# Performance work log

Hardware: AMD Instinct MI355X
Metric: run time of the kernel (lower is better)

## Reference

```python
import jax, jax.numpy as jnp
import numpy as np

E, T, D_IN, D_HID, D_OUT = 8, 2048, 1024, 4096, 1024
INTER = 2 * D_HID  # gated (SwiGLU) -> weight1 produces [gate, val]


def setup_inputs() -> dict:
    key = jax.random.key(0)
    k_x, k_w1, k_w2 = jax.random.split(key, 3)
    # kaiming_uniform-ish scale for weights
    x = jax.random.normal(k_x, (E, T, D_IN), dtype=jnp.float32)
    w1 = jax.random.normal(k_w1, (E, D_IN, INTER), dtype=jnp.float32) * (1.0 / np.sqrt(D_IN))
    w2 = jax.random.normal(k_w2, (E, D_HID, D_OUT), dtype=jnp.float32) * (1.0 / np.sqrt(D_HID))
    return {"x": x, "weight1": w1, "weight2": w2}


def reference(x, weight1, weight2):
    # h: [E, T, 2*D_HID] grouped GEMM over experts
    h = jnp.einsum("etd,edi->eti", x, weight1)
    gate, val = jnp.split(h, 2, axis=-1)
    h = jax.nn.silu(gate) * val  # SwiGLU; dropout is identity in eval / p=0
    out = jnp.einsum("eth,eho->eto", h, weight2)  # [E, T, D_OUT]
    return out
```

## Files before the change

### kernel.cpp

```cpp
#include <hip/hip_runtime.h>


#define E_    8
#define T_    2048
#define DIN   1024
#define DHID  4096
#define DOUT  1024
#define INTER 8192

typedef _Float16 f16;
typedef _Float16 f16x8 __attribute__((ext_vector_type(8)));
typedef float    f32x4 __attribute__((ext_vector_type(4)));

typedef const __attribute__((address_space(1))) void gvoid_t;
typedef __attribute__((address_space(3))) void lvoid_t;

__device__ __forceinline__ void gload_lds16(const void* g, void* l) {
  __builtin_amdgcn_global_load_lds((gvoid_t*)g, (lvoid_t*)l, 16, 0, 0);
}

__global__ __launch_bounds__(256) void conv_f32_f16(
    const float* __restrict__ src, f16* __restrict__ dst, int n8) {
  int i = blockIdx.x * 256 + threadIdx.x;
  int stride = gridDim.x * 256;
  for (; i < n8; i += stride) {
    const float4* s = (const float4*)(src + (size_t)i * 8);
    float4 a0 = s[0], a1 = s[1];
    f16x8 v;
    v[0] = (f16)a0.x; v[1] = (f16)a0.y; v[2] = (f16)a0.z; v[3] = (f16)a0.w;
    v[4] = (f16)a1.x; v[5] = (f16)a1.y; v[6] = (f16)a1.z; v[7] = (f16)a1.w;
    *(f16x8*)(dst + (size_t)i * 8) = v;
  }
}

__global__ __launch_bounds__(256) void xpose64_f32_f16(
    const float* __restrict__ src, f16* __restrict__ dst,
    int R, int C, int tC) {
  __shared__ f16 tile[64][72];
  int bid = blockIdx.x;
  int perE = (R >> 6) * tC;
  int e = bid / perE;
  int rem = bid - e * perE;
  int rt = rem / tC;
  int ct = rem - rt * tC;
  int r0 = rt << 6, c0 = ct << 6;
  int t = threadIdx.x;
  int lr  = t >> 2;
  int lc4 = (t & 3) * 16;
  const float* s = src + (size_t)e * R * C + (size_t)(r0 + lr) * C + c0 + lc4;
#pragma unroll
  for (int i = 0; i < 4; ++i) {
    float4 v = *(const float4*)(s + i * 4);
    tile[lr][lc4 + i * 4 + 0] = (f16)v.x;
    tile[lr][lc4 + i * 4 + 1] = (f16)v.y;
    tile[lr][lc4 + i * 4 + 2] = (f16)v.z;
    tile[lr][lc4 + i * 4 + 3] = (f16)v.w;
  }
  __syncthreads();
  f16* d = dst + (size_t)e * C * R + (size_t)(c0 + lr) * R + r0 + lc4;
  f16x8 o0, o1;
#pragma unroll
  for (int j = 0; j < 8; ++j) o0[j] = tile[lc4 + j][lr];
#pragma unroll
  for (int j = 0; j < 8; ++j) o1[j] = tile[lc4 + 8 + j][lr];
  *(f16x8*)(d)     = o0;
  *(f16x8*)(d + 8) = o1;
}

__global__ __launch_bounds__(512, 2) void gemm1_swiglu_xh(
    const f16* __restrict__ xh,
    const f16* __restrict__ w1t,
    f16* __restrict__ hact) {
  __shared__ f16 As[128][32];
  __shared__ f16 Bg[128][32];
  __shared__ f16 Bv[128][32];

  int bid = blockIdx.x;
  int e   = bid >> 9;
  int rem = bid & 511;
  int mt  = rem >> 5;
  int nt  = rem & 31;
  int m0 = mt * 128, n0 = nt * 128;

  const f16* xe = xh  + ((size_t)e * T_ + m0) * DIN;
  const f16* wg = w1t + ((size_t)e * INTER + n0) * DIN;
  const f16* wv = w1t + ((size_t)e * INTER + DHID + n0) * DIN;

  int tid  = threadIdx.x;
  int lane = tid & 63;
  int wid  = tid >> 6;

  int srow = wid * 16 + (lane >> 2);
  int scol = (lane & 3) * 8;
  f16* lA = &As[wid * 16][0];
  f16* lG = &Bg[wid * 16][0];
  f16* lV = &Bv[wid * 16][0];

  int wm = wid >> 2;
  int wn = wid & 3;
  int lr = lane & 15;
  int lk = (lane >> 4) * 8;

  f32x4 accG[4][2], accV[4][2];
#pragma unroll
  for (int m = 0; m < 4; ++m)
#pragma unroll
    for (int n = 0; n < 2; ++n) {
      accG[m][n] = f32x4{0.f, 0.f, 0.f, 0.f};
      accV[m][n] = f32x4{0.f, 0.f, 0.f, 0.f};
    }

  for (int k = 0; k < DIN; k += 32) {
    __syncthreads();
    gload_lds16(xe + (size_t)srow * DIN + k + scol, lA);
    gload_lds16(wg + (size_t)srow * DIN + k + scol, lG);
    gload_lds16(wv + (size_t)srow * DIN + k + scol, lV);
    __syncthreads();

    f16x8 af[4], bg[2], bv[2];
#pragma unroll
    for (int m = 0; m < 4; ++m)
      af[m] = *(const f16x8*)&As[wm * 64 + m * 16 + lr][lk];
#pragma unroll
    for (int n = 0; n < 2; ++n) {
      bg[n] = *(const f16x8*)&Bg[wn * 32 + n * 16 + lr][lk];
      bv[n] = *(const f16x8*)&Bv[wn * 32 + n * 16 + lr][lk];
    }
#pragma unroll
    for (int m = 0; m < 4; ++m)
#pragma unroll
      for (int n = 0; n < 2; ++n) {
        accG[m][n] = __builtin_amdgcn_mfma_f32_16x16x32_f16(af[m], bg[n], accG[m][n], 0, 0, 0);
        accV[m][n] = __builtin_amdgcn_mfma_f32_16x16x32_f16(af[m], bv[n], accV[m][n], 0, 0, 0);
      }
  }

  f16* he = hact + (size_t)e * T_ * DHID;
  int rbase = m0 + wm * 64 + (lane >> 4) * 4;
  int cbase = n0 + wn * 32 + lr;
#pragma unroll
  for (int m = 0; m < 4; ++m)
#pragma unroll
    for (int n = 0; n < 2; ++n)
#pragma unroll
      for (int j = 0; j < 4; ++j) {
        int row = rbase + m * 16 + j;
        int col = cbase + n * 16;
        float g = accG[m][n][j];
        float v = accV[m][n][j];
        float s = g / (1.0f + __expf(-g));
        he[(size_t)row * DHID + col] = (f16)(s * v);
      }
}

__global__ __launch_bounds__(512, 2) void gemm1_swiglu_rs(
    const float* __restrict__ x,
    const f16* __restrict__ w1t,
    f16* __restrict__ hact) {
  __shared__ f16 As[128][36];
  __shared__ f16 Bg[128][32];
  __shared__ f16 Bv[128][32];

  int bid = blockIdx.x;
  int e   = bid >> 9;
  int rem = bid & 511;
  int mt  = rem >> 5;
  int nt  = rem & 31;
  int m0 = mt * 128, n0 = nt * 128;

  const float* xe = x   + ((size_t)e * T_ + m0) * DIN;
  const f16*   wg = w1t + ((size_t)e * INTER + n0) * DIN;
  const f16*   wv = w1t + ((size_t)e * INTER + DHID + n0) * DIN;

  int tid  = threadIdx.x;
  int lane = tid & 63;
  int wid  = tid >> 6;

  int arow = tid >> 2;
  int acol = (tid & 3) * 8;
  int brow = wid * 16 + (lane >> 2);
  int bcol = (lane & 3) * 8;
  f16* lG = &Bg[wid * 16][0];
  f16* lV = &Bv[wid * 16][0];

  int wm = wid >> 2;
  int wn = wid & 3;
  int lr = lane & 15;
  int lk = (lane >> 4) * 8;

  f32x4 accG[4][2], accV[4][2];
#pragma unroll
  for (int m = 0; m < 4; ++m)
#pragma unroll
    for (int n = 0; n < 2; ++n) {
      accG[m][n] = f32x4{0.f, 0.f, 0.f, 0.f};
      accV[m][n] = f32x4{0.f, 0.f, 0.f, 0.f};
    }

  for (int k = 0; k < DIN; k += 32) {
    __syncthreads();
    gload_lds16(wg + (size_t)brow * DIN + k + bcol, lG);
    gload_lds16(wv + (size_t)brow * DIN + k + bcol, lV);
    {
      const float* sa = xe + (size_t)arow * DIN + k + acol;
      float4 a0 = ((const float4*)sa)[0];
      float4 a1 = ((const float4*)sa)[1];
      f16x8 v;
      v[0] = (f16)a0.x; v[1] = (f16)a0.y; v[2] = (f16)a0.z; v[3] = (f16)a0.w;
      v[4] = (f16)a1.x; v[5] = (f16)a1.y; v[6] = (f16)a1.z; v[7] = (f16)a1.w;
      *(f16x8*)&As[arow][acol] = v;
    }
    __syncthreads();

    f16x8 af[4], bg[2], bv[2];
#pragma unroll
    for (int m = 0; m < 4; ++m)
      af[m] = *(const f16x8*)&As[wm * 64 + m * 16 + lr][lk];
#pragma unroll
    for (int n = 0; n < 2; ++n) {
      bg[n] = *(const f16x8*)&Bg[wn * 32 + n * 16 + lr][lk];
      bv[n] = *(const f16x8*)&Bv[wn * 32 + n * 16 + lr][lk];
    }
#pragma unroll
    for (int m = 0; m < 4; ++m)
#pragma unroll
      for (int n = 0; n < 2; ++n) {
        accG[m][n] = __builtin_amdgcn_mfma_f32_16x16x32_f16(af[m], bg[n], accG[m][n], 0, 0, 0);
        accV[m][n] = __builtin_amdgcn_mfma_f32_16x16x32_f16(af[m], bv[n], accV[m][n], 0, 0, 0);
      }
  }

  f16* he = hact + (size_t)e * T_ * DHID;
  int rbase = m0 + wm * 64 + (lane >> 4) * 4;
  int cbase = n0 + wn * 32 + lr;
#pragma unroll
  for (int m = 0; m < 4; ++m)
#pragma unroll
    for (int n = 0; n < 2; ++n)
#pragma unroll
      for (int j = 0; j < 4; ++j) {
        int row = rbase + m * 16 + j;
        int col = cbase + n * 16;
        float g = accG[m][n][j];
        float v = accV[m][n][j];
        float s = g / (1.0f + __expf(-g));
        he[(size_t)row * DHID + col] = (f16)(s * v);
      }
}

__global__ __launch_bounds__(512, 2) void gemm2_8ph(
    const f16* __restrict__ hact,
    const f16* __restrict__ w2t,
    float* __restrict__ out) {
  __shared__ __align__(1024) f16 As[2][256][64];
  __shared__ __align__(1024) f16 Bs[2][256][64];

  int bid = blockIdx.x;
  int e   = bid >> 5;
  int rem = bid & 31;
  int mt  = rem >> 2;
  int nt  = rem & 3;
  int m0 = mt * 256, n0 = nt * 256;

  const f16* ha = hact + ((size_t)e * T_ + m0) * DHID;
  const f16* wb = w2t  + ((size_t)e * DOUT + n0) * DHID;

  int tid  = threadIdx.x;
  int lane = tid & 63;
  int wid  = tid >> 6;
  int wm   = wid >> 2;
  int wn   = wid & 3;
  int lr   = lane & 15;
  int l16  = lane >> 4;

  int srow = lane >> 3;
  int scol = ((lane & 7) ^ srow) * 8;

  auto stA = [&](int buf, int kt, int i) {
    int ci = wid + 8 * i;
    gload_lds16(ha + (size_t)(ci * 8 + srow) * DHID + kt * 64 + scol,
                (char*)&As[buf][0][0] + ci * 1024);
  };
  auto stB = [&](int buf, int kt, int i) {
    int ci = wid + 8 * i;
    gload_lds16(wb + (size_t)(ci * 8 + srow) * DHID + kt * 64 + scol,
                (char*)&Bs[buf][0][0] + ci * 1024);
  };

  f32x4 acc[8][4];
#pragma unroll
  for (int m = 0; m < 8; ++m)
#pragma unroll
    for (int n = 0; n < 4; ++n) acc[m][n] = f32x4{0.f, 0.f, 0.f, 0.f};

  f16x8 af[4][2], bf0[2][2], bf1[2][2];

#define READ_A2(b, MH)                                                       \
  _Pragma("unroll") for (int m = 0; m < 4; ++m)                              \
  _Pragma("unroll") for (int kk = 0; kk < 2; ++kk) {                         \
    int row_ = wm * 128 + (MH) * 64 + m * 16 + lr;                           \
    af[m][kk] = *(const f16x8*)((const char*)&As[b][0][0] + row_ * 128 +     \
                                (((kk * 4 + l16) ^ (lr & 7)) << 4));         \
  }
#define READ_B2(b, NH, DST)                                                  \
  _Pragma("unroll") for (int n = 0; n < 2; ++n)                              \
  _Pragma("unroll") for (int kk = 0; kk < 2; ++kk) {                         \
    int row_ = wn * 64 + (NH) * 32 + n * 16 + lr;                            \
    DST[n][kk] = *(const f16x8*)((const char*)&Bs[b][0][0] + row_ * 128 +    \
                                 (((kk * 4 + l16) ^ (lr & 7)) << 4));        \
  }
#define MFMA16Q(MH, NH, BB)                                                  \
  __builtin_amdgcn_s_setprio(1);                                            \
  _Pragma("unroll") for (int m = 0; m < 4; ++m)                              \
  _Pragma("unroll") for (int n = 0; n < 2; ++n)                              \
  _Pragma("unroll") for (int kk = 0; kk < 2; ++kk)                          \
    acc[(MH) * 4 + m][(NH) * 2 + n] = __builtin_amdgcn_mfma_f32_16x16x32_f16(\
        af[m][kk], BB[n][kk], acc[(MH) * 4 + m][(NH) * 2 + n], 0, 0, 0);     \
  __builtin_amdgcn_s_setprio(0);
#define BAR() __builtin_amdgcn_s_barrier()
#define LGKM0() asm volatile("s_waitcnt lgkmcnt(0)" ::: "memory")
#define VM6() asm volatile("s_waitcnt vmcnt(6)" ::: "memory")

  stA(0, 0, 0); stA(0, 0, 1); stA(0, 0, 2); stA(0, 0, 3);
  stB(0, 0, 0); stB(0, 0, 1); stB(0, 0, 2); stB(0, 0, 3);
  stB(1, 1, 0); stB(1, 1, 1); stB(1, 1, 2); stB(1, 1, 3);
  stA(1, 1, 0); stA(1, 1, 1);
  VM6();
  BAR();

  for (int it = 0; it < 32; ++it) {
    int tb = 2 * it + 1;
    int pa = (2 * it + 2) & 63;
    int pb = (2 * it + 3) & 63;

    READ_A2(0, 0); READ_B2(0, 0, bf0);
    stA(1, tb, 2); stA(1, tb, 3);
    BAR(); LGKM0();
    MFMA16Q(0, 0, bf0);
    BAR();

    READ_B2(0, 1, bf1);
    BAR(); LGKM0();
    MFMA16Q(0, 1, bf1);
    BAR();

    READ_A2(0, 1);
    stB(0, pa, 0); stB(0, pa, 1);
    BAR(); LGKM0();
    MFMA16Q(1, 0, bf0);
    BAR();

    stB(0, pa, 2); stB(0, pa, 3);
    stA(0, pa, 0); stA(0, pa, 1);
    BAR();
    MFMA16Q(1, 1, bf1);
    VM6();
    BAR();

    READ_A2(1, 0); READ_B2(1, 0, bf0);
    stA(0, pa, 2); stA(0, pa, 3);
    BAR(); LGKM0();
    MFMA16Q(0, 0, bf0);
    BAR();

    READ_B2(1, 1, bf1);
    BAR(); LGKM0();
    MFMA16Q(0, 1, bf1);
    BAR();

    READ_A2(1, 1);
    stB(1, pb, 0); stB(1, pb, 1);
    BAR(); LGKM0();
    MFMA16Q(1, 0, bf0);
    BAR();

    stB(1, pb, 2); stB(1, pb, 3);
    stA(1, pb, 0); stA(1, pb, 1);
    BAR();
    MFMA16Q(1, 1, bf1);
    VM6();
    BAR();
  }

#undef READ_A2
#undef READ_B2
#undef MFMA16Q
#undef BAR
#undef LGKM0
#undef VM6

  float* oe = out + (size_t)e * T_ * DOUT;
  int rbase = m0 + wm * 128 + l16 * 4;
  int cbase = n0 + wn * 64 + lr;
#pragma unroll
  for (int m = 0; m < 8; ++m)
#pragma unroll
    for (int n = 0; n < 4; ++n)
#pragma unroll
      for (int j = 0; j < 4; ++j) {
        int row = rbase + m * 16 + j;
        int col = cbase + n * 16;
        oe[(size_t)row * DOUT + col] = acc[m][n][j];
      }
}

extern "C" void kernel_launch(void* const* d_in, const int* in_sizes, int n_in,
                              void* d_out, int out_size, void* d_ws, size_t ws_size,
                              hipStream_t stream) {
  const float* x  = (const float*)d_in[0];
  const float* w1 = (const float*)d_in[1];
  const float* w2 = (const float*)d_in[2];
  float* out = (float*)d_out;

  const size_t HACT_B = (size_t)E_ * T_ * DHID * 2;
  const size_t WT_B   = (size_t)E_ * INTER * DIN * 2;
  const size_t XH_B   = (size_t)E_ * T_ * DIN * 2;

  f16* hact = (f16*)d_ws;
  f16* wt   = (f16*)((char*)d_ws + HACT_B);

  xpose64_f32_f16<<<E_ * (DIN / 64) * (INTER / 64), 256, 0, stream>>>(
      w1, wt, DIN, INTER, INTER / 64);

  if (ws_size >= HACT_B + WT_B + XH_B) {
    f16* xxh = (f16*)((char*)d_ws + HACT_B + WT_B);
    conv_f32_f16<<<2048, 256, 0, stream>>>(x, xxh, E_ * T_ * DIN / 8);
    gemm1_swiglu_xh<<<E_ * 16 * 32, 512, 0, stream>>>(xxh, wt, hact);
  } else {
    gemm1_swiglu_rs<<<E_ * 16 * 32, 512, 0, stream>>>(x, wt, hact);
  }

  xpose64_f32_f16<<<E_ * (DHID / 64) * (DOUT / 64), 256, 0, stream>>>(
      w2, wt, DHID, DOUT, DOUT / 64);
  gemm2_8ph<<<E_ * 8 * 4, 512, 0, stream>>>(hact, wt, out);
}
```

Before: 600.6 us.

## Double K-tile depth to 64 with XOR-swizzled LDS layout in gemm1

Widens the per-iteration K tile in the gated first GEMM from 32 to 64, halving the number of barrier pairs per output tile. The LDS layout is XOR-swizzled on 16-byte chunks so that MFMA operand reads from 128-byte rows avoid bank conflicts. LDS use doubles to 48KB per block, which may limit the two-blocks-per-CU occupancy target, and loads are still not double-buffered.

After: 564.5 us. 1.06x faster.

```diff
diff --git a/kernel.cpp b/kernel.cpp
--- a/kernel.cpp
+++ b/kernel.cpp
@@ -71,9 +71,9 @@
     const f16* __restrict__ xh,
     const f16* __restrict__ w1t,
     f16* __restrict__ hact) {
-  __shared__ f16 As[128][32];
-  __shared__ f16 Bg[128][32];
-  __shared__ f16 Bv[128][32];
+  __shared__ __align__(1024) f16 As[128][64];
+  __shared__ __align__(1024) f16 Bg[128][64];
+  __shared__ __align__(1024) f16 Bv[128][64];
 
   int bid = blockIdx.x;
   int e   = bid >> 9;
@@ -90,16 +90,29 @@
   int lane = tid & 63;
   int wid  = tid >> 6;
 
-  int srow = wid * 16 + (lane >> 2);
-  int scol = (lane & 3) * 8;
-  f16* lA = &As[wid * 16][0];
-  f16* lG = &Bg[wid * 16][0];
-  f16* lV = &Bv[wid * 16][0];
-
-  int wm = wid >> 2;
-  int wn = wid & 3;
-  int lr = lane & 15;
-  int lk = (lane >> 4) * 8;
+  int srow8 = lane >> 3;
+  int scol  = ((lane & 7) ^ srow8) * 8;
+
+  auto stA = [&](int kt, int i) {
+    int ci = wid + 8 * i;
+    gload_lds16(xe + (size_t)(ci * 8 + srow8) * DIN + kt * 64 + scol,
+                (char*)&As[0][0] + ci * 1024);
+  };
+  auto stG = [&](int kt, int i) {
+    int ci = wid + 8 * i;
+    gload_lds16(wg + (size_t)(ci * 8 + srow8) * DIN + kt * 64 + scol,
+                (char*)&Bg[0][0] + ci * 1024);
+  };
+  auto stV = [&](int kt, int i) {
+    int ci = wid + 8 * i;
+    gload_lds16(wv + (size_t)(ci * 8 + srow8) * DIN + kt * 64 + scol,
+                (char*)&Bv[0][0] + ci * 1024);
+  };
+
+  int wm  = wid >> 2;
+  int wn  = wid & 3;
+  int lr  = lane & 15;
+  int l16 = lane >> 4;
 
   f32x4 accG[4][2], accV[4][2];
 #pragma unroll
@@ -110,33 +123,45 @@
       accV[m][n] = f32x4{0.f, 0.f, 0.f, 0.f};
     }
 
-  for (int k = 0; k < DIN; k += 32) {
+  for (int kt = 0; kt < DIN / 64; ++kt) {
     __syncthreads();
-    gload_lds16(xe + (size_t)srow * DIN + k + scol, lA);
-    gload_lds16(wg + (size_t)srow * DIN + k + scol, lG);
-    gload_lds16(wv + (size_t)srow * DIN + k + scol, lV);
+    stA(kt, 0); stA(kt, 1);
+    stG(kt, 0); stG(kt, 1);
+    stV(kt, 0); stV(kt, 1);
     __syncthreads();
 
-    f16x8 af[4], bg[2], bv[2];
+    f16x8 af[4][2], bg[2][2], bv[2][2];
 #pragma unroll
     for (int m = 0; m < 4; ++m)
-      af[m] = *(const f16x8*)&As[wm * 64 + m * 16 + lr][lk];
-#pragma unroll
-    for (int n = 0; n < 2; ++n) {
-      bg[n] = *(const f16x8*)&Bg[wn * 32 + n * 16 + lr][lk];
-      bv[n] = *(const f16x8*)&Bv[wn * 32 + n * 16 + lr][lk];
-    }
+#pragma unroll
+      for (int kk = 0; kk < 2; ++kk) {
+        int row_ = wm * 64 + m * 16 + lr;
+        af[m][kk] = *(const f16x8*)((const char*)&As[0][0] + row_ * 128 +
+                                    (((kk * 4 + l16) ^ (lr & 7)) << 4));
+      }
+#pragma unroll
+    for (int n = 0; n < 2; ++n)
+#pragma unroll
+      for (int kk = 0; kk < 2; ++kk) {
+        int row_ = wn * 32 + n * 16 + lr;
+        bg[n][kk] = *(const f16x8*)((const char*)&Bg[0][0] + row_ * 128 +
+                                    (((kk * 4 + l16) ^ (lr & 7)) << 4));
+        bv[n][kk] = *(const f16x8*)((const char*)&Bv[0][0] + row_ * 128 +
+                                    (((kk * 4 + l16) ^ (lr & 7)) << 4));
+      }
 #pragma unroll
     for (int m = 0; m < 4; ++m)
 #pragma unroll
-      for (int n = 0; n < 2; ++n) {
-        accG[m][n] = __builtin_amdgcn_mfma_f32_16x16x32_f16(af[m], bg[n], accG[m][n], 0, 0, 0);
-        accV[m][n] = __builtin_amdgcn_mfma_f32_16x16x32_f16(af[m], bv[n], accV[m][n], 0, 0, 0);
-      }
+      for (int n = 0; n < 2; ++n)
+#pragma unroll
+        for (int kk = 0; kk < 2; ++kk) {
+          accG[m][n] = __builtin_amdgcn_mfma_f32_16x16x32_f16(af[m][kk], bg[n][kk], accG[m][n], 0, 0, 0);
+          accV[m][n] = __builtin_amdgcn_mfma_f32_16x16x32_f16(af[m][kk], bv[n][kk], accV[m][n], 0, 0, 0);
+        }
   }
 
   f16* he = hact + (size_t)e * T_ * DHID;
-  int rbase = m0 + wm * 64 + (lane >> 4) * 4;
+  int rbase = m0 + wm * 64 + l16 * 4;
   int cbase = n0 + wn * 32 + lr;
 #pragma unroll
   for (int m = 0; m < 4; ++m)
```
